# Optimization experiments

Hardware: AMD Instinct MI355X
Metric: run time of the kernel (lower is better)

The kernel has to match this reference:

```python
import jax, jax.numpy as jnp
import numpy as np

B, FI, FO, K, DIM_STYLE, H, W = 8, 512, 512, 3, 512, 64, 64
EPS = 1e-8


def setup_inputs() -> dict:
    key = jax.random.key(0)
    ks = jax.random.split(key, 5)
    return {
        "x": jax.random.normal(ks[0], (B, FI, H, W), dtype=jnp.float32),
        "style": jax.random.normal(ks[1], (B, DIM_STYLE), dtype=jnp.float32),
        "w": jax.random.normal(ks[2], (FO, FI, K, K), dtype=jnp.float32),
        "mod_w": jax.random.normal(ks[3], (FI, DIM_STYLE), dtype=jnp.float32),
        "mod_b": jax.random.normal(ks[4], (FI,), dtype=jnp.float32),
    }


def _fir_filter(dtype):
    # upfirdn2d.setup_filter([1,3,3,1]): normalize 1D to sum 1, outer product -> 4x4, sum 1
    f1 = jnp.array([1.0, 3.0, 3.0, 1.0], dtype=dtype)
    f1 = f1 / jnp.sum(f1)
    f = jnp.outer(f1, f1)
    # gain = up**2 = 4 applied inside upfirdn2d; filter is symmetric so flip is a no-op
    return (f * 4.0)[::-1, ::-1]


def _mod_conv_up(x, style, w, mod_w, mod_b):
    # modLinear: F.linear(style, mod_w * dim_style**-0.5, bias=mod_b)
    s = style @ (mod_w * (DIM_STYLE ** -0.5)).T + mod_b  # [B, FI]
    # modulate: w_scale * style broadcast over input channels
    w_scale = (FI * K * K) ** -0.5
    wm = w[None] * (w_scale * s[:, None, :, None, None])  # [B, FO, FI, K, K]
    # demodulate
    demod = jax.lax.rsqrt(jnp.sum(wm * wm, axis=(2, 3, 4)) + EPS)  # [B, FO]
    wm = wm * demod[:, :, None, None, None]
    # conv2d_resample up=2 fast path == conv_transpose2d(stride=2, padding=0) per sample,
    def tconv(xs, ws):  # xs [FI,H,W], ws [FO,FI,K,K]
        y = jax.lax.conv_general_dilated(
            xs[None], ws[:, :, ::-1, ::-1],
            window_strides=(1, 1), padding=[(K - 1, K - 1), (K - 1, K - 1)],
            lhs_dilation=(2, 2),
            dimension_numbers=("NCHW", "OIHW", "NCHW"))
        return y[0]

    y = jax.vmap(tconv)(x, wm)  # [B, FO, 2H+1, 2W+1]
    # FIR low-pass: upfirdn2d(pad=[1,1,1,1], gain=4) -> output [B, FO, 2H, 2W]
    f = _fir_filter(y.dtype)
    Bn, C, Hh, Ww = y.shape
    yf = y.reshape(Bn * C, 1, Hh, Ww)
    yf = jax.lax.conv_general_dilated(
        yf, f[None, None], window_strides=(1, 1), padding=[(1, 1), (1, 1)],
        dimension_numbers=("NCHW", "OIHW", "NCHW"))
    return yf.reshape(Bn, C, Hh - 1, Ww - 1)


def reference(x, style, w, mod_w, mod_b):
    return _mod_conv_up(x, style, w, mod_w, mod_b)
```

## Files before the change

### kernel.cpp

```cpp
#include <hip/hip_runtime.h>

typedef _Float16 f16;
typedef f16 f16x8 __attribute__((ext_vector_type(8)));
typedef float f32x4 __attribute__((ext_vector_type(4)));

#define OFF_SMOD  0u
#define OFF_SSQ   16384u
#define OFF_DEMOD 32768u
#define OFF_WSQ   49152u
#define OFF_WPAR  1097728u
#define OFF_XP    5816320u
#define XP_BYTES  35685376u
#define OFF_YP    41501696u
#define PLANE     4560

__global__ void style_kernel(const float* __restrict__ style, const float* __restrict__ mod_w,
                             const float* __restrict__ mod_b, float* __restrict__ smod,
                             float* __restrict__ ssq) {
    int b = blockIdx.x;
    int fi = threadIdx.x;
    __shared__ float st[512];
    st[fi] = style[b * 512 + fi];
    __syncthreads();
    float sum = 0.f;
    const float* mw = mod_w + (size_t)fi * 512;
    for (int d = 0; d < 512; ++d) sum += st[d] * mw[d];
    float s = sum * 0.04419417382415922f  + mod_b[fi];
    smod[b * 512 + fi] = s * 0.014731391274719741f ;
    ssq[b * 512 + fi] = s * s;
}

__global__ void wsq_kernel(const float* __restrict__ w, float* __restrict__ wsq) {
    int fo = blockIdx.x;
    int fi = threadIdx.x;
    const float* p = w + ((size_t)fo * 512 + fi) * 9;
    float s = 0.f;
#pragma unroll
    for (int k = 0; k < 9; ++k) { float v = p[k]; s += v * v; }
    wsq[fo * 512 + fi] = s;
}

__global__ void demod_kernel(const float* __restrict__ ssq, const float* __restrict__ wsq,
                             float* __restrict__ demod) {
    int b = blockIdx.x >> 1;
    int fo = (blockIdx.x & 1) * 256 + threadIdx.x;
    __shared__ float sq[512];
    for (int i = threadIdx.x; i < 512; i += 256) sq[i] = ssq[b * 512 + i];
    __syncthreads();
    float sum = 0.f;
    const float* wr = wsq + (size_t)fo * 512;
    for (int fi = 0; fi < 512; ++fi) sum += sq[fi] * wr[fi];
    demod[b * 512 + fo] = rsqrtf(sum * (1.0f / 4608.0f) + 1e-8f);
}

__global__ void xp_kernel(const float* __restrict__ x, const float* __restrict__ smod,
                          f16* __restrict__ xp) {
    int id = blockIdx.x;
    int fc = id & 7;
    int h = (id >> 3) & 63;
    int b = id >> 9;
    int fi0 = fc * 64;
    __shared__ f16 tile[64 * 65];
    int tid = threadIdx.x;
#pragma unroll
    for (int it = 0; it < 16; ++it) {
        int e = it * 256 + tid;
        int i = e >> 6, wc = e & 63;
        float v = x[(((size_t)(b * 512 + fi0 + i)) * 64 + h) * 64 + wc];
        tile[i * 65 + wc] = (f16)(v * smod[b * 512 + fi0 + i]);
    }
    __syncthreads();
#pragma unroll
    for (int it = 0; it < 16; ++it) {
        int e = it * 256 + tid;
        int wc = e >> 6, i = e & 63;
        xp[((size_t)(b * 4356 + (h + 1) * 66 + (wc + 1))) * 512 + fi0 + i] = tile[i * 65 + wc];
    }
}

__global__ void wpar2_kernel(const float* __restrict__ w, f16* __restrict__ wpar2) {
    const int wi_[9] = {8, 6, 2, 0, 7, 1, 5, 3, 4};
    int fo = blockIdx.x;
#pragma unroll
    for (int half = 0; half < 2; ++half) {
        int fi = half * 256 + threadIdx.x;
        const float* p = w + ((size_t)fo * 512 + fi) * 9;
        int fc = fi >> 5, ch = fi & 31;
#pragma unroll
        for (int s = 0; s < 9; ++s)
            wpar2[(((size_t)s * 16 + fc) * 512 + fo) * 32 + ch] = (f16)p[wi_[s]];
    }
}

__global__ void ring2_kernel(f16* __restrict__ P) {
    int idx = blockIdx.x * 256 + threadIdx.x;
    if (idx >= 16384 * 133) return;
    int slab = idx / 133, r = idx - slab * 133;
    f16* base = P + (size_t)slab * PLANE;
    if (r < 68) base[r] = (f16)0.f;
    else base[(r - 67) * 68] = (f16)0.f;
}

template <int C>
__device__ __forceinline__ void tconv_body(const f16* __restrict__ wpar2, const f16* __restrict__ xp,
                                           f16* __restrict__ P, f16* Xs, int b, int fg, int n0t) {
    constexpr int NT   = (C == 0) ? 4 : (C == 3) ? 1 : 2;
    constexpr int SB   = (C == 0) ? 0 : (C == 1) ? 4 : (C == 2) ? 6 : 8;
    constexpr int LB   = (C <= 1) ? 67 : (C == 2) ? 1 : 0;
    constexpr int WOFF = (C <= 1) ? 0 : (C == 2) ? 66 : 67;
    constexpr int WLEN = (C <= 1) ? 195 : (C == 2) ? 129 : 128;
    constexpr int CH4  = WLEN * 4;
    constexpr int CH4P = (CH4 + 7) & ~7;
    constexpr int Q    = 16 * NT;
    constexpr int offs[4] = {(C == 0) ? -67 : (C == 1) ? -66 : (C == 2) ? -1 : 0,
                             (C == 0) ? -66 : 0, -1, 0};

    int tid = threadIdx.x, lane = tid & 63, wave = tid >> 6;
    int wm = wave >> 1, wn = wave & 1, kb = lane >> 4, lr = lane & 15;
    int n0 = n0t << 7, fo0 = fg << 7;
    int WB = b * 4356 + n0 + WOFF;
    int bmax = b * 4356 + 4356;

    f32x4 acc[4][4];
#pragma unroll
    for (int m = 0; m < 4; ++m)
#pragma unroll
        for (int n = 0; n < 4; ++n) acc[m][n] = (f32x4){0.f, 0.f, 0.f, 0.f};

    int4 xr2[2][4];
    f16x8 afr[3][4], bfr[2][4];

    const f16* abase = wpar2 + ((size_t)(fo0 + wm * 64 + lr)) * 32 + (size_t)kb * 8;
    auto loadA = [&](int q, f16x8* dst) {
        int fc = q / NT, tap = q - fc * NT;
        const f16* p = abase + (size_t)((SB + tap) * 16 + fc) * (512 * 32);
#pragma unroll
        for (int m = 0; m < 4; ++m) dst[m] = *(const f16x8*)(p + m * 16 * 32);
    };
    auto loadX = [&](int k, int4* xr) {
        int fi0 = k * 32;
#pragma unroll
        for (int it = 0; it < 4; ++it) {
            int idx = it * 256 + tid;
            int4 v = {0, 0, 0, 0};
            if (idx < CH4) {
                int r = idx >> 2, part = idx & 3;
                int pr = WB + r;
                if (pr <= bmax) v = *(const int4*)(xp + ((size_t)pr * 512 + fi0 + part * 8));
            }
            xr[it] = v;
        }
    };
    auto writeX = [&](int buf, const int4* xr) {
#pragma unroll
        for (int it = 0; it < 4; ++it) {
            int idx = it * 256 + tid;
            if (idx < CH4) {
                int r = idx >> 2, part = idx & 3;
                *(int4*)((char*)Xs + buf * (CH4P * 16) + (((r * 4 + part) ^ (r & 7)) << 4)) = xr[it];
            }
        }
    };
    auto readBF = [&](int buf, int tap, f16x8* dst) {
#pragma unroll
        for (int n = 0; n < 4; ++n) {
            int r = wn * 64 + n * 16 + lr + offs[tap] + LB;
            dst[n] = *(const f16x8*)((const char*)Xs + buf * (CH4P * 16) + (((r * 4 + kb) ^ (r & 7)) << 4));
        }
    };

    loadX(0, xr2[0]);
    loadA(0, afr[0]);
    loadA(1, afr[1 % 3]);
    writeX(0, xr2[0]);
    __syncthreads();
    loadX(1, xr2[1]);
    readBF(0, 0, bfr[0]);

#pragma unroll
    for (int k = 0; k < 16; ++k) {
        const int cur = k & 1;
        if (k < 14) loadX(k + 2, xr2[k & 1]);
        if (k < 15) writeX(1 - cur, xr2[(k + 1) & 1]);
#pragma unroll
        for (int tap = 0; tap < NT - 1; ++tap) {
            const int q = k * NT + tap;
            if (q + 2 < Q) loadA(q + 2, afr[(q + 2) % 3]);
            readBF(cur, tap + 1, bfr[(q + 1) & 1]);
            __builtin_amdgcn_s_setprio(1);
#pragma unroll
            for (int m = 0; m < 4; ++m)
#pragma unroll
                for (int n = 0; n < 4; ++n)
                    acc[m][n] = __builtin_amdgcn_mfma_f32_16x16x32_f16(afr[q % 3][m], bfr[q & 1][n], acc[m][n], 0, 0, 0);
            __builtin_amdgcn_s_setprio(0);
        }
        {
            const int q = k * NT + NT - 1;
            if (k < 15) __syncthreads();
            if (q + 2 < Q) loadA(q + 2, afr[(q + 2) % 3]);
            if (k < 15) readBF(1 - cur, 0, bfr[(q + 1) & 1]);
            __builtin_amdgcn_s_setprio(1);
#pragma unroll
            for (int m = 0; m < 4; ++m)
#pragma unroll
                for (int n = 0; n < 4; ++n)
                    acc[m][n] = __builtin_amdgcn_mfma_f32_16x16x32_f16(afr[q % 3][m], bfr[q & 1][n], acc[m][n], 0, 0, 0);
            __builtin_amdgcn_s_setprio(0);
        }
    }

    size_t slab = (size_t)(C * 8 + b) * 512;
#pragma unroll
    for (int m = 0; m < 4; ++m) {
#pragma unroll
        for (int j = 0; j < 4; ++j) {
            int fo = fo0 + wm * 64 + m * 16 + kb * 4 + j;
            f16* pb = P + (slab + fo) * PLANE;
#pragma unroll
            for (int n = 0; n < 4; ++n) {
                int nn = n0 + wn * 64 + n * 16 + lr;
                int t = (nn * 993) >> 16;
                int s = nn - t * 66;
                pb[(t + 1) * 68 + (s + 1)] = (f16)acc[m][n][j];
            }
        }
    }
}

__global__ __launch_bounds__(256, 2) void tconv2_kernel(const f16* __restrict__ wpar2,
                                                        const f16* __restrict__ xp,
                                                        f16* __restrict__ P) {
    __shared__ __align__(16) f16 Xs[2 * 784 * 8];
    int id = blockIdx.x;
    int b = id & 7;
    int r = id >> 3;
    int c = r / 136;
    int r2 = r - c * 136;
    int fg = r2 / 34;
    int n0t = r2 - fg * 34;
    switch (c) {
        case 0: tconv_body<0>(wpar2, xp, P, Xs, b, fg, n0t); break;
        case 1: tconv_body<1>(wpar2, xp, P, Xs, b, fg, n0t); break;
        case 2: tconv_body<2>(wpar2, xp, P, Xs, b, fg, n0t); break;
        default: tconv_body<3>(wpar2, xp, P, Xs, b, fg, n0t); break;
    }
}

__global__ __launch_bounds__(256, 4) void fir3_kernel(const f16* __restrict__ P,
                                                      const float* __restrict__ demod,
                                                      float* __restrict__ out) {
    int bid = blockIdx.x;
    int b = bid & 7, fo = bid >> 3;
    __shared__ __align__(16) f16 yr[4][4488];
    const size_t pstep = (size_t)8 * 512 * PLANE;
    int tid = threadIdx.x;
    const f16* src0 = P + ((size_t)(b * 512 + fo)) * PLANE;
#pragma unroll
    for (int c = 0; c < 4; ++c) {
        const int4* src = (const int4*)(src0 + c * pstep);
        int4* dst = (int4*)(&yr[c][0]);
#pragma unroll
        for (int it = 0; it < 3; ++it) {
            int idx = it * 256 + tid;
            if (idx < 561) dst[idx] = src[idx];
        }
    }
    __syncthreads();
    float dm = demod[b * 512 + fo];
    int OX = tid & 127, rg = tid >> 7;
    int OYb = rg * 64;
    int e = OX & 1;
    int c0o = (1 - e) * 4488 + (((OX - 1) >> 1) + 1);
    int c1o = e * 4488 + ((OX >> 1) + 1);
    int c2o = (1 - e) * 4488 + (((OX + 1) >> 1) + 1);
    int c3o = e * 4488 + (((OX + 2) >> 1) + 1);
    const f16* yf = &yr[0][0];
    size_t obase = ((size_t)(b * 512 + fo)) * 16384 + OX;
    float h0 = 0.f, h1 = 0.f, h2 = 0.f, h3 = 0.f;
#pragma unroll 4
    for (int i = 0; i < 67; ++i) {
        int oy = OYb - 1 + i;
        int base = (oy & 1) * (2 * 4488) + ((oy >> 1) + 1) * 68;
        float h = 0.25f * ((float)yf[base + c0o] + (float)yf[base + c3o])
                + 0.75f * ((float)yf[base + c1o] + (float)yf[base + c2o]);
        h0 = h1; h1 = h2; h2 = h3; h3 = h;
        if (i >= 3) {
            float a = 0.25f * (h0 + h3) + 0.75f * (h1 + h2);
            out[obase + (size_t)(OYb + i - 3) * 128] = a * dm;
        }
    }
}

extern "C" void kernel_launch(void* const* d_in, const int* in_sizes, int n_in,
                              void* d_out, int out_size, void* d_ws, size_t ws_size,
                              hipStream_t stream) {
    const float* x = (const float*)d_in[0];
    const float* style = (const float*)d_in[1];
    const float* w = (const float*)d_in[2];
    const float* mod_w = (const float*)d_in[3];
    const float* mod_b = (const float*)d_in[4];
    float* out = (float*)d_out;

    char* ws = (char*)d_ws;
    float* smod = (float*)(ws + OFF_SMOD);
    float* ssq = (float*)(ws + OFF_SSQ);
    float* demod = (float*)(ws + OFF_DEMOD);
    float* wsq = (float*)(ws + OFF_WSQ);
    f16* wpar2 = (f16*)(ws + OFF_WPAR);
    f16* xp = (f16*)(ws + OFF_XP);
    f16* P = (f16*)(ws + OFF_YP);

    style_kernel<<<8, 512, 0, stream>>>(style, mod_w, mod_b, smod, ssq);
    wsq_kernel<<<512, 512, 0, stream>>>(w, wsq);
    demod_kernel<<<16, 256, 0, stream>>>(ssq, wsq, demod);
    wpar2_kernel<<<512, 256, 0, stream>>>(w, wpar2);
    hipMemsetAsync(xp, 0, XP_BYTES, stream);
    xp_kernel<<<4096, 256, 0, stream>>>(x, smod, xp);
    ring2_kernel<<<8512, 256, 0, stream>>>(P);
    tconv2_kernel<<<4352, 256, 0, stream>>>(wpar2, xp, P);
    fir3_kernel<<<4096, 256, 0, stream>>>(P, demod, out);
}
```

Baseline: 423.8 us.

## Share one X tile across all four parity classes within a 512-thread block

Replaces the per-parity-class tconv blocks with 512-thread blocks in which 8 waves split the four output parity classes and two 64-row filter halves. All waves share a single 132-row staged input tile per 32-channel slice, loaded once instead of once per class. Input staging moves to a triple-buffered LDS ring with one barrier per k-step. This cuts redundant global and LDS traffic for X, but puts waves with unequal tap counts (4/2/2/1) behind a shared barrier, so they can stall on each other.

```diff
diff --git a/kernel.cpp b/kernel.cpp
--- a/kernel.cpp
+++ b/kernel.cpp
@@ -102,24 +102,17 @@
 }
 
 template <int C>
-__device__ __forceinline__ void tconv_body(const f16* __restrict__ wpar2, const f16* __restrict__ xp,
-                                           f16* __restrict__ P, f16* Xs, int b, int fg, int n0t) {
-    constexpr int NT   = (C == 0) ? 4 : (C == 3) ? 1 : 2;
-    constexpr int SB   = (C == 0) ? 0 : (C == 1) ? 4 : (C == 2) ? 6 : 8;
-    constexpr int LB   = (C <= 1) ? 67 : (C == 2) ? 1 : 0;
-    constexpr int WOFF = (C <= 1) ? 0 : (C == 2) ? 66 : 67;
-    constexpr int WLEN = (C <= 1) ? 195 : (C == 2) ? 129 : 128;
-    constexpr int CH4  = WLEN * 4;
-    constexpr int CH4P = (CH4 + 7) & ~7;
-    constexpr int Q    = 16 * NT;
-    constexpr int offs[4] = {(C == 0) ? -67 : (C == 1) ? -66 : (C == 2) ? -1 : 0,
-                             (C == 0) ? -66 : 0, -1, 0};
-
-    int tid = threadIdx.x, lane = tid & 63, wave = tid >> 6;
-    int wm = wave >> 1, wn = wave & 1, kb = lane >> 4, lr = lane & 15;
-    int n0 = n0t << 7, fo0 = fg << 7;
-    int WB = b * 4356 + n0 + WOFF;
-    int bmax = b * 4356 + 4356;
+__device__ __forceinline__ void tconv3_body(const f16* __restrict__ wpar2, const f16* __restrict__ xp,
+                                            f16* __restrict__ P, f16* Xs, int b, int fo0, int n0, int h) {
+    constexpr int NT = (C == 0) ? 4 : (C == 3) ? 1 : 2;
+    constexpr int SB = (C == 0) ? 0 : (C == 1) ? 4 : (C == 2) ? 6 : 8;
+    constexpr int DELT[4] = {(C == 0) ? 0 : (C == 1) ? 1 : (C == 2) ? 66 : 67,
+                             (C == 0) ? 1 : 67, 66, 67};
+
+    int tid = threadIdx.x, lane = tid & 63;
+    int kb = lane >> 4, lr = lane & 15;
+    int wbase = b * 4356 + n0;
+    int rmax = 4356 - n0;
 
     f32x4 acc[4][4];
 #pragma unroll
@@ -127,87 +120,74 @@
 #pragma unroll
         for (int n = 0; n < 4; ++n) acc[m][n] = (f32x4){0.f, 0.f, 0.f, 0.f};
 
-    int4 xr2[2][4];
-    f16x8 afr[3][4], bfr[2][4];
-
-    const f16* abase = wpar2 + ((size_t)(fo0 + wm * 64 + lr)) * 32 + (size_t)kb * 8;
-    auto loadA = [&](int q, f16x8* dst) {
-        int fc = q / NT, tap = q - fc * NT;
-        const f16* p = abase + (size_t)((SB + tap) * 16 + fc) * (512 * 32);
+    int4 xr[2];
+    f16x8 afr[2][4], bfr[2][4];
+
+    int u1 = tid, r1 = u1 >> 2, p1 = u1 & 3;
+    bool has2 = tid < 12;
+    int u2 = tid + 512, r2 = u2 >> 2, p2 = u2 & 3;
+    const f16* xrow1 = xp + (size_t)(wbase + r1) * 512 + p1 * 8;
+    const f16* xrow2 = xp + (size_t)(wbase + r2) * 512 + p2 * 8;
+    char* wdst1 = (char*)Xs + ((u1 ^ (r1 & 7)) << 4);
+    char* wdst2 = (char*)Xs + ((u2 ^ (r2 & 7)) << 4);
+    bool v1 = r1 <= rmax;
+    bool v2 = has2 && (r2 <= rmax);
+
+    auto loadX = [&](int k) {
+        int off = k * 32;
+        int4 a = {0, 0, 0, 0}, c2 = {0, 0, 0, 0};
+        if (v1) a = *(const int4*)(xrow1 + off);
+        if (v2) c2 = *(const int4*)(xrow2 + off);
+        xr[0] = a; xr[1] = c2;
+    };
+    auto writeX = [&](int buf) {
+        *(int4*)(wdst1 + buf * 8448) = xr[0];
+        if (has2) *(int4*)(wdst2 + buf * 8448) = xr[1];
+    };
+    auto loadA = [&](int sl, int kk, f16x8* dst) {
+        const f16* p = wpar2 + ((size_t)(sl * 16 + kk) * 512 + fo0 + h * 64 + lr) * 32 + kb * 8;
 #pragma unroll
         for (int m = 0; m < 4; ++m) dst[m] = *(const f16x8*)(p + m * 16 * 32);
     };
-    auto loadX = [&](int k, int4* xr) {
-        int fi0 = k * 32;
-#pragma unroll
-        for (int it = 0; it < 4; ++it) {
-            int idx = it * 256 + tid;
-            int4 v = {0, 0, 0, 0};
-            if (idx < CH4) {
-                int r = idx >> 2, part = idx & 3;
-                int pr = WB + r;
-                if (pr <= bmax) v = *(const int4*)(xp + ((size_t)pr * 512 + fi0 + part * 8));
+    auto readBF = [&](int buf, int delt, f16x8* dst) {
+#pragma unroll
+        for (int nf = 0; nf < 4; ++nf) {
+            int rr = nf * 16 + lr + delt;
+            dst[nf] = *(const f16x8*)((const char*)Xs + buf * 8448 + (((rr * 4 + kb) ^ (rr & 7)) << 4));
+        }
+    };
+
+    loadX(0);
+    writeX(0);
+    loadX(1);
+    loadA(SB, 0, afr[0]);
+
+#pragma unroll 6
+    for (int k = 0; k < 16; ++k) {
+        if (k < 15) {
+            writeX((k + 1) % 3);
+            if (k < 14) loadX(k + 2);
+            __syncthreads();
+        }
+        const int cur = k % 3;
+        readBF(cur, DELT[0], bfr[(k * NT) & 1]);
+#pragma unroll
+        for (int tap = 0; tap < NT; ++tap) {
+            const int q = k * NT + tap;
+            if (tap + 1 < NT) {
+                loadA(SB + tap + 1, k, afr[(q + 1) & 1]);
+                readBF(cur, DELT[tap + 1], bfr[(q + 1) & 1]);
+            } else if (k < 15) {
+                loadA(SB, k + 1, afr[(q + 1) & 1]);
             }
-            xr[it] = v;
-        }
-    };
-    auto writeX = [&](int buf, const int4* xr) {
-#pragma unroll
-        for (int it = 0; it < 4; ++it) {
-            int idx = it * 256 + tid;
-            if (idx < CH4) {
-                int r = idx >> 2, part = idx & 3;
-                *(int4*)((char*)Xs + buf * (CH4P * 16) + (((r * 4 + part) ^ (r & 7)) << 4)) = xr[it];
-            }
-        }
-    };
-    auto readBF = [&](int buf, int tap, f16x8* dst) {
-#pragma unroll
-        for (int n = 0; n < 4; ++n) {
-            int r = wn * 64 + n * 16 + lr + offs[tap] + LB;
-            dst[n] = *(const f16x8*)((const char*)Xs + buf * (CH4P * 16) + (((r * 4 + kb) ^ (r & 7)) << 4));
-        }
-    };
-
-    loadX(0, xr2[0]);
-    loadA(0, afr[0]);
-    loadA(1, afr[1 % 3]);
-    writeX(0, xr2[0]);
-    __syncthreads();
-    loadX(1, xr2[1]);
-    readBF(0, 0, bfr[0]);
-
-#pragma unroll
-    for (int k = 0; k < 16; ++k) {
-        const int cur = k & 1;
-        if (k < 14) loadX(k + 2, xr2[k & 1]);
-        if (k < 15) writeX(1 - cur, xr2[(k + 1) & 1]);
-#pragma unroll
-        for (int tap = 0; tap < NT - 1; ++tap) {
-            const int q = k * NT + tap;
-            if (q + 2 < Q) loadA(q + 2, afr[(q + 2) % 3]);
-            readBF(cur, tap + 1, bfr[(q + 1) & 1]);
             __builtin_amdgcn_s_setprio(1);
 #pragma unroll
             for (int m = 0; m < 4; ++m)
 #pragma unroll
-                for (int n = 0; n < 4; ++n)
-                    acc[m][n] = __builtin_amdgcn_mfma_f32_16x16x32_f16(afr[q % 3][m], bfr[q & 1][n], acc[m][n], 0, 0, 0);
+                for (int nf = 0; nf < 4; ++nf)
+                    acc[m][nf] = __builtin_amdgcn_mfma_f32_16x16x32_f16(afr[q & 1][m], bfr[q & 1][nf], acc[m][nf], 0, 0, 0);
             __builtin_amdgcn_s_setprio(0);
         }
-        {
-            const int q = k * NT + NT - 1;
-            if (k < 15) __syncthreads();
-            if (q + 2 < Q) loadA(q + 2, afr[(q + 2) % 3]);
-            if (k < 15) readBF(1 - cur, 0, bfr[(q + 1) & 1]);
-            __builtin_amdgcn_s_setprio(1);
-#pragma unroll
-            for (int m = 0; m < 4; ++m)
-#pragma unroll
-                for (int n = 0; n < 4; ++n)
-                    acc[m][n] = __builtin_amdgcn_mfma_f32_16x16x32_f16(afr[q % 3][m], bfr[q & 1][n], acc[m][n], 0, 0, 0);
-            __builtin_amdgcn_s_setprio(0);
-        }
     }
 
     size_t slab = (size_t)(C * 8 + b) * 512;
@@ -215,35 +195,37 @@
     for (int m = 0; m < 4; ++m) {
 #pragma unroll
         for (int j = 0; j < 4; ++j) {
-            int fo = fo0 + wm * 64 + m * 16 + kb * 4 + j;
+            int fo = fo0 + h * 64 + m * 16 + kb * 4 + j;
             f16* pb = P + (slab + fo) * PLANE;
 #pragma unroll
-            for (int n = 0; n < 4; ++n) {
-                int nn = n0 + wn * 64 + n * 16 + lr;
+            for (int nf = 0; nf < 4; ++nf) {
+                int nn = n0 + nf * 16 + lr;
                 int t = (nn * 993) >> 16;
                 int s = nn - t * 66;
-                pb[(t + 1) * 68 + (s + 1)] = (f16)acc[m][n][j];
+                pb[(t + 1) * 68 + (s + 1)] = (f16)acc[m][nf][j];
             }
         }
     }
 }
 
-__global__ __launch_bounds__(256, 2) void tconv2_kernel(const f16* __restrict__ wpar2,
+__global__ __launch_bounds__(512, 2) void tconv3_kernel(const f16* __restrict__ wpar2,
                                                         const f16* __restrict__ xp,
                                                         f16* __restrict__ P) {
-    __shared__ __align__(16) f16 Xs[2 * 784 * 8];
+    __shared__ __align__(16) f16 Xs[3 * 528 * 8];
     int id = blockIdx.x;
     int b = id & 7;
     int r = id >> 3;
-    int c = r / 136;
-    int r2 = r - c * 136;
-    int fg = r2 / 34;
-    int n0t = r2 - fg * 34;
+    int fg = r / 68;
+    int n0t = r - fg * 68;
+    int fo0 = fg << 7, n0 = n0t << 6;
+    int w = threadIdx.x >> 6;
+    int h = w >> 2;
+    int c = (w == 0 || w == 5) ? 0 : (w == 2 || w == 7) ? 1 : (w == 3 || w == 6) ? 2 : 3;
     switch (c) {
-        case 0: tconv_body<0>(wpar2, xp, P, Xs, b, fg, n0t); break;
-        case 1: tconv_body<1>(wpar2, xp, P, Xs, b, fg, n0t); break;
-        case 2: tconv_body<2>(wpar2, xp, P, Xs, b, fg, n0t); break;
-        default: tconv_body<3>(wpar2, xp, P, Xs, b, fg, n0t); break;
+        case 0: tconv3_body<0>(wpar2, xp, P, Xs, b, fo0, n0, h); break;
+        case 1: tconv3_body<1>(wpar2, xp, P, Xs, b, fo0, n0, h); break;
+        case 2: tconv3_body<2>(wpar2, xp, P, Xs, b, fo0, n0, h); break;
+        default: tconv3_body<3>(wpar2, xp, P, Xs, b, fo0, n0, h); break;
     }
 }
 
@@ -318,6 +300,6 @@
     hipMemsetAsync(xp, 0, XP_BYTES, stream);
     xp_kernel<<<4096, 256, 0, stream>>>(x, smod, xp);
     ring2_kernel<<<8512, 256, 0, stream>>>(P);
-    tconv2_kernel<<<4352, 256, 0, stream>>>(wpar2, xp, P);
+    tconv3_kernel<<<2176, 512, 0, stream>>>(wpar2, xp, P);
     fir3_kernel<<<4096, 256, 0, stream>>>(P, demod, out);
 }
```

Measured after the change: 452.5 us. 1.07x slower.
